# Kernel optimization log

Measured on AMD Instinct MI355X. Metric: run time of the kernel, lower is better.

Reference implementation:

```python
import jax, jax.numpy as jnp
import numpy as np

N_NODES = 100000
N_EDGES = 3200000  # avg degree 32
EPS = 1e-12


def setup_inputs() -> dict:
    key = jax.random.key(0)
    k1, k2, k3, k4, k5 = jax.random.split(key, 5)
    positions = jax.random.normal(k1, (N_NODES, 3), dtype=jnp.float32)
    node_feat = jnp.ones((N_NODES, 1), dtype=jnp.float32)  # dummy 1x0e data
    w0 = jax.random.normal(k2, (1,), dtype=jnp.float32)    # linear weight for 0e output
    w1 = jax.random.normal(k3, (3,), dtype=jnp.float32)    # linear weight for 1o output (elementwise)
    edge_src = jax.random.randint(k4, (N_EDGES,), 0, N_NODES, dtype=jnp.int32)
    edge_dst = jax.random.randint(k5, (N_EDGES,), 0, N_NODES, dtype=jnp.int32)
    return {"positions": positions, "node_feat": node_feat, "w0": w0, "w1": w1,
            "edge_src": edge_src, "edge_dst": edge_dst}


def reference(positions, node_feat, w0, w1, edge_src, edge_dst):
    n_nodes = positions.shape[0]
    # relative positions per edge: dest - src  [E,3]
    rel = positions[edge_dst] - positions[edge_src]
    # spherical harmonics lmax=1: Y0 = 1 (constant 0e), Y1 = unit direction (1o)
    norm = jnp.sqrt(jnp.sum(rel * rel, axis=-1, keepdims=True))
    sh1 = rel / jnp.maximum(norm, EPS)                      # [E,3]
    # gather dest-node scalar feature (code gathers dest_node_feat)
    s = node_feat[edge_dst]                                 # [E,1]
    # tensor product of 0e scalar with (0e + 1o): tp0 = s*1, tp1 = s*sh1
    # LinearLayer: elementwise multiply by per-irrep weight vectors
    out0 = w0 * s                                           # [E,1]
    out1 = w1 * (s * sh1)                                   # [E,3]
    edge_out = jnp.concatenate([out0, out1], axis=-1)       # [E,4]
    # scatter-mean aggregation over incoming edges per dest node
    sums = jax.ops.segment_sum(edge_out, edge_dst, num_segments=n_nodes)
    ones = jnp.ones((edge_out.shape[0], 1), dtype=edge_out.dtype)
    counts = jax.ops.segment_sum(ones, edge_dst, num_segments=n_nodes)
    return sums / jnp.maximum(counts, 1.0)                  # [N,4]
```

## Files before the change

### kernel.cpp

```cpp
#include <hip/hip_runtime.h>


#define EPS 1e-12f
#define FSCALE 128.0f
#define FBIAS 128
#define CHUNK_SHIFT 11
#define CHUNK 2048
#define NCHUNK_MAX 64
#define BLKA 512
#define TPA 8
#define NSTAGE (BLKA * TPA)
#define BLKB 512
#define SHARDS 8

__global__ void repack_pos(const float* __restrict__ pos,
                           float4* __restrict__ pos4,
                           unsigned* __restrict__ gcnt,
                           int n_nodes, int padded) {
    int n = blockIdx.x * blockDim.x + threadIdx.x;
    if (n < SHARDS * NCHUNK_MAX) gcnt[n] = 0;
    if (n >= padded) return;
    float4 p = make_float4(0.f, 0.f, 0.f, 0.f);
    if (n < n_nodes) {
        p.x = pos[3 * n + 0];
        p.y = pos[3 * n + 1];
        p.z = pos[3 * n + 2];
    }
    pos4[n] = p;
}

__global__ __launch_bounds__(BLKA) void phaseA(
        const int* __restrict__ dst,
        const int* __restrict__ src,
        unsigned* __restrict__ gcnt,
        unsigned* __restrict__ recs,
        int n_edges, int capx, int n_chunk) {
    __shared__ unsigned stage[NSTAGE];
    __shared__ unsigned h[NCHUNK_MAX];
    __shared__ unsigned pref[NCHUNK_MAX + 1];
    __shared__ unsigned gbase[NCHUNK_MAX];
    int tid = threadIdx.x;
    int shard = (int)blockIdx.x & (SHARDS - 1);
    if (tid < n_chunk) h[tid] = 0;
    __syncthreads();

    long e0 = (long)blockIdx.x * NSTAGE;
    unsigned rec[TPA];
    int ch[TPA];
    unsigned rank[TPA];
    bool val[TPA];
#pragma unroll
    for (int t = 0; t < TPA; ++t) {
        long j = e0 + (long)t * BLKA + tid;
        val[t] = (j < n_edges);
        if (val[t]) {
            int d = dst[j];
            int s = src[j];
            ch[t] = d >> CHUNK_SHIFT;
            rec[t] = ((unsigned)(d & (CHUNK - 1)) << 17) | (unsigned)s;
            rank[t] = atomicAdd(&h[ch[t]], 1u);
        }
    }
    __syncthreads();
    if (tid < 64) {
        unsigned v = (tid < n_chunk) ? h[tid] : 0u;
#pragma unroll
        for (int ofs = 1; ofs < 64; ofs <<= 1) {
            unsigned u = __shfl_up(v, ofs, 64);
            if (tid >= ofs) v += u;
        }
        if (tid == 0) pref[0] = 0;
        if (tid < n_chunk) pref[tid + 1] = v;
    }
    if (tid < n_chunk)
        gbase[tid] = h[tid] ? atomicAdd(&gcnt[shard * NCHUNK_MAX + tid], h[tid]) : 0u;
    __syncthreads();
#pragma unroll
    for (int t = 0; t < TPA; ++t)
        if (val[t]) stage[pref[ch[t]] + rank[t]] = rec[t];
    __syncthreads();
    unsigned total = pref[n_chunk];
    for (unsigned i = tid; i < total; i += BLKA) {
        int lo = 0, hi = n_chunk - 1;
        while (lo < hi) {
            int mid = (lo + hi + 1) >> 1;
            if (pref[mid] <= i) lo = mid; else hi = mid - 1;
        }
        unsigned idx = gbase[lo] + (i - pref[lo]);
        if (idx < (unsigned)capx)
            recs[(size_t)(shard * n_chunk + lo) * (unsigned)capx + idx] = stage[i];
    }
}

__global__ __launch_bounds__(BLKB) void phaseB(
        const unsigned* __restrict__ gcnt,
        const unsigned* __restrict__ recs,
        const float4* __restrict__ pos4,
        unsigned long long* __restrict__ accR,
        int capx, int n_chunk, int padded) {
    __shared__ unsigned long long acc[CHUNK];
    __shared__ float4 posw[CHUNK];
    int c     = (int)blockIdx.x % n_chunk;
    int shard = (int)blockIdx.x / n_chunk;
    int base  = c << CHUNK_SHIFT;

    for (int i = threadIdx.x; i < CHUNK; i += BLKB) {
        acc[i] = 0ull;
        posw[i] = pos4[base + i];
    }
    __syncthreads();

    unsigned cnt = gcnt[shard * NCHUNK_MAX + c];
    if (cnt > (unsigned)capx) cnt = (unsigned)capx;
    const unsigned* bucket = recs + (size_t)(shard * n_chunk + c) * (unsigned)capx;
    for (unsigned j = threadIdx.x; j < cnt; j += BLKB) {
        unsigned r = bucket[j];
        unsigned s = r & 0x1FFFFu;
        unsigned local = r >> 17;
        float4 ps = pos4[s];
        float4 pd = posw[local];
        float rx = pd.x - ps.x;
        float ry = pd.y - ps.y;
        float rz = pd.z - ps.z;
        float inv = 1.0f / fmaxf(sqrtf(rx * rx + ry * ry + rz * rz), EPS);
        unsigned fx = (unsigned)(FBIAS + (int)rintf(rx * inv * FSCALE));
        unsigned fy = (unsigned)(FBIAS + (int)rintf(ry * inv * FSCALE));
        unsigned fz = (unsigned)(FBIAS + (int)rintf(rz * inv * FSCALE));
        unsigned long long p = ((unsigned long long)fx << 48)
                             | ((unsigned long long)fy << 32)
                             | ((unsigned long long)fz << 16) | 1ull;
        atomicAdd(&acc[local], p);
    }
    __syncthreads();

    unsigned long long* row = accR + (size_t)shard * (unsigned)padded + base;
    for (int i = threadIdx.x; i < CHUNK; i += BLKB) row[i] = acc[i];
}

__global__ void finalize_binned(const unsigned long long* __restrict__ accR,
                                const float* __restrict__ feat,
                                const float* __restrict__ w0,
                                const float* __restrict__ w1,
                                float* __restrict__ out,
                                int n_nodes, int padded) {
    int n = blockIdx.x * blockDim.x + threadIdx.x;
    if (n >= n_nodes) return;
    int Fx = 0, Fy = 0, Fz = 0, C = 0;
    for (int s = 0; s < SHARDS; ++s) {
        unsigned long long v = accR[(size_t)s * (unsigned)padded + (unsigned)n];
        Fx += (int)(v >> 48);
        Fy += (int)((v >> 32) & 0xffffull);
        Fz += (int)((v >> 16) & 0xffffull);
        C  += (int)(v & 0xffffull);
    }
    float c = (float)C;
    float rd = 1.0f / fmaxf(c, 1.0f);
    float sx = (float)Fx * (1.0f / FSCALE) - c;
    float sy = (float)Fy * (1.0f / FSCALE) - c;
    float sz = (float)Fz * (1.0f / FSCALE) - c;
    float f = feat[n];
    float4 o;
    o.x = w0[0] * f * c * rd;
    o.y = w1[0] * f * sx * rd;
    o.z = w1[1] * f * sy * rd;
    o.w = w1[2] * f * sz * rd;
    ((float4*)out)[n] = o;
}

__global__ void edge_kernel_agent(const float* __restrict__ pos,
                                  const int* __restrict__ dst,
                                  const int* __restrict__ src,
                                  unsigned long long* __restrict__ acc,
                                  int n_edges, int n_nodes, int rmask) {
    int i = blockIdx.x * blockDim.x + threadIdx.x;
    if (i >= n_edges) return;
    int s = src[i];
    int d = dst[i];
    float rx = pos[3 * d + 0] - pos[3 * s + 0];
    float ry = pos[3 * d + 1] - pos[3 * s + 1];
    float rz = pos[3 * d + 2] - pos[3 * s + 2];
    float inv = 1.0f / fmaxf(sqrtf(rx * rx + ry * ry + rz * rz), EPS);
    unsigned fx = (unsigned)(FBIAS + (int)rintf(rx * inv * FSCALE));
    unsigned fy = (unsigned)(FBIAS + (int)rintf(ry * inv * FSCALE));
    unsigned fz = (unsigned)(FBIAS + (int)rintf(rz * inv * FSCALE));
    unsigned long long p = ((unsigned long long)fx << 48)
                         | ((unsigned long long)fy << 32)
                         | ((unsigned long long)fz << 16) | 1ull;
    unsigned r = (unsigned)blockIdx.x & (unsigned)rmask;
    atomicAdd(acc + (size_t)r * (unsigned)n_nodes + (unsigned)d, p);
}

__global__ void finalize_flat(const unsigned long long* __restrict__ acc,
                              const float* __restrict__ feat,
                              const float* __restrict__ w0,
                              const float* __restrict__ w1,
                              float* __restrict__ out,
                              int n_nodes, int R) {
    int n = blockIdx.x * blockDim.x + threadIdx.x;
    if (n >= n_nodes) return;
    int Fx = 0, Fy = 0, Fz = 0, C = 0;
    for (int r = 0; r < R; ++r) {
        unsigned long long v = acc[(size_t)r * n_nodes + n];
        Fx += (int)(v >> 48);
        Fy += (int)((v >> 32) & 0xffffull);
        Fz += (int)((v >> 16) & 0xffffull);
        C  += (int)(v & 0xffffull);
    }
    float c = (float)C;
    float rd = 1.0f / fmaxf(c, 1.0f);
    float sx = (float)Fx * (1.0f / FSCALE) - c;
    float sy = (float)Fy * (1.0f / FSCALE) - c;
    float sz = (float)Fz * (1.0f / FSCALE) - c;
    float f = feat[n];
    float4 o;
    o.x = w0[0] * f * c * rd;
    o.y = w1[0] * f * sx * rd;
    o.z = w1[1] * f * sy * rd;
    o.w = w1[2] * f * sz * rd;
    ((float4*)out)[n] = o;
}

extern "C" void kernel_launch(void* const* d_in, const int* in_sizes, int n_in,
                              void* d_out, int out_size, void* d_ws, size_t ws_size,
                              hipStream_t stream) {
    const float* pos  = (const float*)d_in[0];
    const float* feat = (const float*)d_in[1];
    const float* w0   = (const float*)d_in[2];
    const float* w1   = (const float*)d_in[3];
    const int* esrc   = (const int*)d_in[4];
    const int* edst   = (const int*)d_in[5];
    int n_nodes = in_sizes[0] / 3;
    int n_edges = in_sizes[4];

    int n_chunk = (n_nodes + CHUNK - 1) >> CHUNK_SHIFT;
    int padded  = n_chunk * CHUNK;
    int capx = (int)((long)n_edges / ((long)SHARDS * n_chunk) + 1024);

    size_t off_pos4 = 0;
    size_t pos4_bytes = (size_t)padded * sizeof(float4);
    size_t off_gcnt = (pos4_bytes + 255) & ~(size_t)255;
    size_t gcnt_bytes = (size_t)SHARDS * NCHUNK_MAX * sizeof(unsigned);
    size_t off_recs = off_gcnt + ((gcnt_bytes + 255) & ~(size_t)255);
    size_t recs_bytes = (size_t)SHARDS * n_chunk * (unsigned)capx * sizeof(unsigned);
    size_t off_accR = off_recs + ((recs_bytes + 255) & ~(size_t)255);
    size_t accR_bytes = (size_t)SHARDS * (unsigned)padded * sizeof(unsigned long long);
    size_t need = off_accR + accR_bytes;

    int nb = 256;
    int ng = (n_nodes + nb - 1) / nb;

    if (n_chunk <= NCHUNK_MAX && n_nodes <= (1 << 17) && ws_size >= need) {
        float4* pos4 = (float4*)((char*)d_ws + off_pos4);
        unsigned* gcnt = (unsigned*)((char*)d_ws + off_gcnt);
        unsigned* recs = (unsigned*)((char*)d_ws + off_recs);
        unsigned long long* accR = (unsigned long long*)((char*)d_ws + off_accR);

        int rg = (padded + nb - 1) / nb;
        repack_pos<<<rg, nb, 0, stream>>>(pos, pos4, gcnt, n_nodes, padded);

        int ga = (int)((n_edges + (long)NSTAGE - 1) / (long)NSTAGE);
        phaseA<<<ga, BLKA, 0, stream>>>(edst, esrc, gcnt, recs,
                                        n_edges, capx, n_chunk);
        phaseB<<<n_chunk * SHARDS, BLKB, 0, stream>>>(gcnt, recs, pos4, accR,
                                                      capx, n_chunk, padded);
        finalize_binned<<<ng, nb, 0, stream>>>(accR, feat, w0, w1,
                                               (float*)d_out, n_nodes, padded);
    } else {
        int R = 4;
        while (R > 1 && (size_t)R * n_nodes * sizeof(unsigned long long) > ws_size) R >>= 1;
        unsigned long long* acc = (unsigned long long*)d_ws;
        hipMemsetAsync(acc, 0, (size_t)R * n_nodes * sizeof(unsigned long long), stream);
        int eb = 256;
        int eg = (n_edges + eb - 1) / eb;
        edge_kernel_agent<<<eg, eb, 0, stream>>>(pos, edst, esrc, acc,
                                                 n_edges, n_nodes, R - 1);
        finalize_flat<<<ng, nb, 0, stream>>>(acc, feat, w0, w1,
                                             (float*)d_out, n_nodes, R);
    }
}
```

Before: 118.5 us.

## Replace global bucket atomics with per-block sorted segments and fuse position repack

Phase A no longer reserves space in global buckets with atomics. Each block writes its locally chunk-sorted records contiguously, plus a table of per-chunk offsets. The position repack moves into phase A, which removes one kernel launch. Phase B now gathers each chunk's records from a range of block segments, finding the segment for each record by binary search over prefix offsets. It also reads destination positions from global memory instead of staging them in shared memory. This drops the global atomics, the capacity clamp and the scattered writes, at the cost of a serial prefix sum and a binary search per record in phase B. It also assumes pos4 is fully written before phase B, which holds only because phase B is a separate launch.

```diff
diff --git a/kernel.cpp b/kernel.cpp
--- a/kernel.cpp
+++ b/kernel.cpp
@@ -11,40 +11,41 @@
 #define TPA 8
 #define NSTAGE (BLKA * TPA)
 #define BLKB 512
-#define SHARDS 8
-
-__global__ void repack_pos(const float* __restrict__ pos,
-                           float4* __restrict__ pos4,
-                           unsigned* __restrict__ gcnt,
-                           int n_nodes, int padded) {
-    int n = blockIdx.x * blockDim.x + threadIdx.x;
-    if (n < SHARDS * NCHUNK_MAX) gcnt[n] = 0;
-    if (n >= padded) return;
-    float4 p = make_float4(0.f, 0.f, 0.f, 0.f);
-    if (n < n_nodes) {
-        p.x = pos[3 * n + 0];
-        p.y = pos[3 * n + 1];
-        p.z = pos[3 * n + 2];
-    }
-    pos4[n] = p;
-}
+#define REPL 8
+#define MAXSEG 160
 
 __global__ __launch_bounds__(BLKA) void phaseA(
+        const float* __restrict__ pos,
         const int* __restrict__ dst,
         const int* __restrict__ src,
-        unsigned* __restrict__ gcnt,
+        float4* __restrict__ pos4,
+        unsigned* __restrict__ boff,
         unsigned* __restrict__ recs,
-        int n_edges, int capx, int n_chunk) {
+        int n_edges, int n_chunk, int n_nodes, int padded) {
     __shared__ unsigned stage[NSTAGE];
     __shared__ unsigned h[NCHUNK_MAX];
     __shared__ unsigned pref[NCHUNK_MAX + 1];
-    __shared__ unsigned gbase[NCHUNK_MAX];
     int tid = threadIdx.x;
-    int shard = (int)blockIdx.x & (SHARDS - 1);
+    int b = (int)blockIdx.x;
+
+    int npb = (padded + (int)gridDim.x - 1) / (int)gridDim.x;
+    for (int i = tid; i < npb; i += BLKA) {
+        int n = b * npb + i;
+        if (n < padded) {
+            float4 p = make_float4(0.f, 0.f, 0.f, 0.f);
+            if (n < n_nodes) {
+                p.x = pos[3 * n + 0];
+                p.y = pos[3 * n + 1];
+                p.z = pos[3 * n + 2];
+            }
+            pos4[n] = p;
+        }
+    }
+
     if (tid < n_chunk) h[tid] = 0;
     __syncthreads();
 
-    long e0 = (long)blockIdx.x * NSTAGE;
+    long e0 = (long)b * NSTAGE;
     unsigned rec[TPA];
     int ch[TPA];
     unsigned rank[TPA];
@@ -72,53 +73,62 @@
         if (tid == 0) pref[0] = 0;
         if (tid < n_chunk) pref[tid + 1] = v;
     }
-    if (tid < n_chunk)
-        gbase[tid] = h[tid] ? atomicAdd(&gcnt[shard * NCHUNK_MAX + tid], h[tid]) : 0u;
-    __syncthreads();
+    __syncthreads();
+    if (tid <= n_chunk) boff[(size_t)b * (n_chunk + 1) + tid] = pref[tid];
 #pragma unroll
     for (int t = 0; t < TPA; ++t)
         if (val[t]) stage[pref[ch[t]] + rank[t]] = rec[t];
     __syncthreads();
     unsigned total = pref[n_chunk];
-    for (unsigned i = tid; i < total; i += BLKA) {
-        int lo = 0, hi = n_chunk - 1;
-        while (lo < hi) {
-            int mid = (lo + hi + 1) >> 1;
-            if (pref[mid] <= i) lo = mid; else hi = mid - 1;
-        }
-        unsigned idx = gbase[lo] + (i - pref[lo]);
-        if (idx < (unsigned)capx)
-            recs[(size_t)(shard * n_chunk + lo) * (unsigned)capx + idx] = stage[i];
-    }
+    unsigned* dstp = recs + (size_t)b * NSTAGE;
+    for (unsigned i = tid; i < total; i += BLKA) dstp[i] = stage[i];
 }
 
 __global__ __launch_bounds__(BLKB) void phaseB(
-        const unsigned* __restrict__ gcnt,
+        const unsigned* __restrict__ boff,
         const unsigned* __restrict__ recs,
         const float4* __restrict__ pos4,
         unsigned long long* __restrict__ accR,
-        int capx, int n_chunk, int padded) {
+        int n_chunk, int padded, int ga) {
     __shared__ unsigned long long acc[CHUNK];
-    __shared__ float4 posw[CHUNK];
-    int c     = (int)blockIdx.x % n_chunk;
-    int shard = (int)blockIdx.x / n_chunk;
-    int base  = c << CHUNK_SHIFT;
-
-    for (int i = threadIdx.x; i < CHUNK; i += BLKB) {
-        acc[i] = 0ull;
-        posw[i] = pos4[base + i];
-    }
-    __syncthreads();
-
-    unsigned cnt = gcnt[shard * NCHUNK_MAX + c];
-    if (cnt > (unsigned)capx) cnt = (unsigned)capx;
-    const unsigned* bucket = recs + (size_t)(shard * n_chunk + c) * (unsigned)capx;
-    for (unsigned j = threadIdx.x; j < cnt; j += BLKB) {
-        unsigned r = bucket[j];
-        unsigned s = r & 0x1FFFFu;
-        unsigned local = r >> 17;
+    __shared__ unsigned segoff[MAXSEG + 1];
+    __shared__ unsigned segbase[MAXSEG];
+    __shared__ unsigned lens[MAXSEG];
+    int tid = threadIdx.x;
+    int c = (int)blockIdx.x % n_chunk;
+    int r = (int)blockIdx.x / n_chunk;
+    int lo = (int)((long)ga * r / REPL);
+    int hi = (int)((long)ga * (r + 1) / REPL);
+    int nseg = hi - lo;
+    int base = c << CHUNK_SHIFT;
+
+    for (int i = tid; i < CHUNK; i += BLKB) acc[i] = 0ull;
+    for (int i = tid; i < nseg; i += BLKB) {
+        unsigned o0 = boff[(size_t)(lo + i) * (n_chunk + 1) + c];
+        unsigned o1 = boff[(size_t)(lo + i) * (n_chunk + 1) + c + 1];
+        lens[i] = o1 - o0;
+        segbase[i] = (unsigned)(lo + i) * NSTAGE + o0;
+    }
+    __syncthreads();
+    if (tid <= nseg) {
+        unsigned a = 0;
+        for (int i = 0; i < tid; ++i) a += lens[i];
+        segoff[tid] = a;
+    }
+    __syncthreads();
+
+    unsigned total = segoff[nseg];
+    for (unsigned i = tid; i < total; i += BLKB) {
+        int s0 = 0, s1 = nseg - 1;
+        while (s0 < s1) {
+            int mid = (s0 + s1 + 1) >> 1;
+            if (segoff[mid] <= i) s0 = mid; else s1 = mid - 1;
+        }
+        unsigned rv = recs[segbase[s0] + (i - segoff[s0])];
+        unsigned s = rv & 0x1FFFFu;
+        unsigned local = rv >> 17;
         float4 ps = pos4[s];
-        float4 pd = posw[local];
+        float4 pd = pos4[base + local];
         float rx = pd.x - ps.x;
         float ry = pd.y - ps.y;
         float rz = pd.z - ps.z;
@@ -133,8 +143,8 @@
     }
     __syncthreads();
 
-    unsigned long long* row = accR + (size_t)shard * (unsigned)padded + base;
-    for (int i = threadIdx.x; i < CHUNK; i += BLKB) row[i] = acc[i];
+    unsigned long long* row = accR + (size_t)r * (unsigned)padded + base;
+    for (int i = tid; i < CHUNK; i += BLKB) row[i] = acc[i];
 }
 
 __global__ void finalize_binned(const unsigned long long* __restrict__ accR,
@@ -146,7 +156,7 @@
     int n = blockIdx.x * blockDim.x + threadIdx.x;
     if (n >= n_nodes) return;
     int Fx = 0, Fy = 0, Fz = 0, C = 0;
-    for (int s = 0; s < SHARDS; ++s) {
+    for (int s = 0; s < REPL; ++s) {
         unsigned long long v = accR[(size_t)s * (unsigned)padded + (unsigned)n];
         Fx += (int)(v >> 48);
         Fy += (int)((v >> 32) & 0xffffull);
@@ -234,35 +244,33 @@
 
     int n_chunk = (n_nodes + CHUNK - 1) >> CHUNK_SHIFT;
     int padded  = n_chunk * CHUNK;
-    int capx = (int)((long)n_edges / ((long)SHARDS * n_chunk) + 1024);
+    int ga = (int)(((long)n_edges + NSTAGE - 1) / NSTAGE);
+    int nseg_max = (ga + REPL - 1) / REPL;
 
     size_t off_pos4 = 0;
     size_t pos4_bytes = (size_t)padded * sizeof(float4);
-    size_t off_gcnt = (pos4_bytes + 255) & ~(size_t)255;
-    size_t gcnt_bytes = (size_t)SHARDS * NCHUNK_MAX * sizeof(unsigned);
-    size_t off_recs = off_gcnt + ((gcnt_bytes + 255) & ~(size_t)255);
-    size_t recs_bytes = (size_t)SHARDS * n_chunk * (unsigned)capx * sizeof(unsigned);
+    size_t off_boff = (pos4_bytes + 255) & ~(size_t)255;
+    size_t boff_bytes = (size_t)ga * (n_chunk + 1) * sizeof(unsigned);
+    size_t off_recs = off_boff + ((boff_bytes + 255) & ~(size_t)255);
+    size_t recs_bytes = (size_t)ga * NSTAGE * sizeof(unsigned);
     size_t off_accR = off_recs + ((recs_bytes + 255) & ~(size_t)255);
-    size_t accR_bytes = (size_t)SHARDS * (unsigned)padded * sizeof(unsigned long long);
+    size_t accR_bytes = (size_t)REPL * (unsigned)padded * sizeof(unsigned long long);
     size_t need = off_accR + accR_bytes;
 
     int nb = 256;
     int ng = (n_nodes + nb - 1) / nb;
 
-    if (n_chunk <= NCHUNK_MAX && n_nodes <= (1 << 17) && ws_size >= need) {
+    if (n_chunk <= NCHUNK_MAX && n_nodes <= (1 << 17) && nseg_max <= MAXSEG
+        && ws_size >= need) {
         float4* pos4 = (float4*)((char*)d_ws + off_pos4);
-        unsigned* gcnt = (unsigned*)((char*)d_ws + off_gcnt);
+        unsigned* boff = (unsigned*)((char*)d_ws + off_boff);
         unsigned* recs = (unsigned*)((char*)d_ws + off_recs);
         unsigned long long* accR = (unsigned long long*)((char*)d_ws + off_accR);
 
-        int rg = (padded + nb - 1) / nb;
-        repack_pos<<<rg, nb, 0, stream>>>(pos, pos4, gcnt, n_nodes, padded);
-
-        int ga = (int)((n_edges + (long)NSTAGE - 1) / (long)NSTAGE);
-        phaseA<<<ga, BLKA, 0, stream>>>(edst, esrc, gcnt, recs,
-                                        n_edges, capx, n_chunk);
-        phaseB<<<n_chunk * SHARDS, BLKB, 0, stream>>>(gcnt, recs, pos4, accR,
-                                                      capx, n_chunk, padded);
+        phaseA<<<ga, BLKA, 0, stream>>>(pos, edst, esrc, pos4, boff, recs,
+                                        n_edges, n_chunk, n_nodes, padded);
+        phaseB<<<n_chunk * REPL, BLKB, 0, stream>>>(boff, recs, pos4, accR,
+                                                    n_chunk, padded, ga);
         finalize_binned<<<ng, nb, 0, stream>>>(accR, feat, w0, w1,
                                                (float*)d_out, n_nodes, padded);
     } else {
```

Result: slower. 123.2 us (+4.0%).
